# Kernel tuning notes

Hardware: AMD Instinct MI355X
Metric: run time of the kernel (lower is better)

## Reference

```python
import jax, jax.numpy as jnp
import numpy as np
from functools import partial

B, S, H, L, NH, V, A, NL = 64, 256, 768, 12, 12, 30522, 64, 2
HD = H // NH
EPS = 1e-12


def _ln(x, s, b):
    m = jnp.mean(x, axis=-1, keepdims=True)
    v = jnp.mean((x - m) ** 2, axis=-1, keepdims=True)
    return (x - m) * jax.lax.rsqrt(v + EPS) * s + b


def setup_inputs() -> dict:
    key = jax.random.key(0)
    ks = jax.random.split(key, 16)
    sc = 0.02
    inp = {
        'input_ids': jax.random.randint(ks[0], (B, S), 0, V, dtype=jnp.int32),
        'attention_mask': jnp.ones((B, S), dtype=jnp.int32),
        'token_type_ids': jnp.zeros((B, S), dtype=jnp.int32),
        'annotator_idx': jax.random.randint(ks[1], (B,), 0, A, dtype=jnp.int32),
        'word_emb': jax.random.normal(ks[2], (V, H), jnp.float32) * sc,
        'pos_emb': jax.random.normal(ks[3], (512, H), jnp.float32) * sc,
        'type_emb': jax.random.normal(ks[4], (2, H), jnp.float32) * sc,
        'emb_ln_s': jnp.ones((H,), jnp.float32),
        'emb_ln_b': jnp.zeros((H,), jnp.float32),
        'Wq': jax.random.normal(ks[5], (L, H, H), jnp.float32) * sc,
        'bq': jnp.zeros((L, H), jnp.float32),
        'Wk': jax.random.normal(ks[6], (L, H, H), jnp.float32) * sc,
        'bk': jnp.zeros((L, H), jnp.float32),
        'Wv': jax.random.normal(ks[7], (L, H, H), jnp.float32) * sc,
        'bv': jnp.zeros((L, H), jnp.float32),
        'Wo': jax.random.normal(ks[8], (L, H, H), jnp.float32) * sc,
        'bo': jnp.zeros((L, H), jnp.float32),
        'ln1_s': jnp.ones((L, H), jnp.float32),
        'ln1_b': jnp.zeros((L, H), jnp.float32),
        'W1': jax.random.normal(ks[9], (L, H, 4 * H), jnp.float32) * sc,
        'b1': jnp.zeros((L, 4 * H), jnp.float32),
        'W2': jax.random.normal(ks[10], (L, 4 * H, H), jnp.float32) * sc,
        'b2': jnp.zeros((L, H), jnp.float32),
        'ln2_s': jnp.ones((L, H), jnp.float32),
        'ln2_b': jnp.zeros((L, H), jnp.float32),
        'head_W': jax.random.normal(ks[11], (A, H, NL), jnp.float32) * sc,
        'head_b': jnp.zeros((A, NL), jnp.float32),
    }
    return inp


def _bert_forward(input_ids, attention_mask, token_type_ids, word_emb, pos_emb,
                  type_emb, emb_ln_s, emb_ln_b, layer_params):
    # embeddings
    h = word_emb[input_ids] + pos_emb[:S][None, :, :] + type_emb[token_type_ids]
    h = _ln(h, emb_ln_s, emb_ln_b)
    # additive attention bias from mask: [B,1,1,S]
    mask_bias = (1.0 - attention_mask.astype(h.dtype))[:, None, None, :] * -10000.0
    scale = 1.0 / np.sqrt(HD)

    def layer(h, p):
        Wq, bq, Wk, bk, Wv, bv, Wo, bo, l1s, l1b, W1, b1, W2, b2, l2s, l2b = p
        def heads(x, W, b):  # [B,S,H] -> [B,NH,S,HD]
            y = x @ W + b
            return y.reshape(B, S, NH, HD).transpose(0, 2, 1, 3)
        q = heads(h, Wq, bq)
        k = heads(h, Wk, bk)
        v = heads(h, Wv, bv)
        scores = jnp.einsum('bhqd,bhkd->bhqk', q, k) * scale + mask_bias
        attn = jax.nn.softmax(scores, axis=-1)
        ctx = jnp.einsum('bhqk,bhkd->bhqd', attn, v)
        ctx = ctx.transpose(0, 2, 1, 3).reshape(B, S, H)
        h = _ln(h + ctx @ Wo + bo, l1s, l1b)
        ffn = jax.nn.gelu(h @ W1 + b1, approximate=False) @ W2 + b2
        h = _ln(h + ffn, l2s, l2b)
        return h, None

    h, _ = jax.lax.scan(layer, h, layer_params)
    return h


def reference(input_ids, attention_mask, token_type_ids, annotator_idx,
              word_emb, pos_emb, type_emb, emb_ln_s, emb_ln_b,
              Wq, bq, Wk, bk, Wv, bv, Wo, bo, ln1_s, ln1_b,
              W1, b1, W2, b2, ln2_s, ln2_b, head_W, head_b):
    layer_params = (Wq, bq, Wk, bk, Wv, bv, Wo, bo, ln1_s, ln1_b,
                    W1, b1, W2, b2, ln2_s, ln2_b)
    h = _bert_forward(input_ids, attention_mask, token_type_ids, word_emb,
                      pos_emb, type_emb, emb_ln_s, emb_ln_b, layer_params)
    cls = h[:, 0, :]  # [B,H]
    # per-sample annotator-head routing: gather head weights, batched matvec
    logits = jnp.einsum('bh,bhl->bl', cls, head_W[annotator_idx]) + head_b[annotator_idx]
    return logits
```

## Files before the change

kernel.cpp:

```cpp
#include <hip/hip_runtime.h>

#define L_ 12
#define H_ 768
#define S_ 256
#define B_ 64
#define NH_ 12
#define HD_ 64
#define FF_ 3072
#define M_ (B_*S_)
#define QKVN (3*H_)

using bf16x8 = __attribute__((ext_vector_type(8))) __bf16;
using floatx4 = __attribute__((ext_vector_type(4))) float;

typedef const __attribute__((address_space(1))) void* gptr_t;
typedef __attribute__((address_space(3))) void* sptr_t;

__device__ __forceinline__ void async_copy16(const void* g, void* s) {
  __builtin_amdgcn_global_load_lds((gptr_t)g, (sptr_t)s, 16, 0, 0);
}

__device__ __forceinline__ unsigned short f2bf(float f) {
  unsigned int u = __float_as_uint(f);
  u += 0x7fffu + ((u >> 16) & 1u);
  return (unsigned short)(u >> 16);
}
__device__ __forceinline__ float bf2f(unsigned short s) {
  return __uint_as_float(((unsigned int)s) << 16);
}

__device__ __forceinline__ float gelu_f(float x) {
  float y = 0.7978845608f * (x + 0.044715f * x * x * x);
  float t = 1.0f - 2.0f / (1.0f + __expf(2.0f * y));
  return 0.5f * x * (1.0f + t);
}

__global__ __launch_bounds__(256) void transpose_bf16_kernel(
    const float* __restrict__ W, unsigned short* __restrict__ Wt, int K, int N) {
  __shared__ unsigned short t[64][65];
  const int n0 = blockIdx.x * 64, k0 = blockIdx.y * 64;
  const int tid = threadIdx.x;
#pragma unroll
  for (int p = 0; p < 16; ++p) {
    int idx = p * 256 + tid;
    int r = idx >> 6, c = idx & 63;
    t[r][c] = f2bf(W[(size_t)(k0 + r) * N + n0 + c]);
  }
  __syncthreads();
#pragma unroll
  for (int p = 0; p < 16; ++p) {
    int idx = p * 256 + tid;
    int r = idx >> 6, c = idx & 63;
    Wt[(size_t)(n0 + r) * K + k0 + c] = t[c][r];
  }
}

__global__ __launch_bounds__(256) void v_transpose_kernel(
    const unsigned short* __restrict__ qkv, unsigned short* __restrict__ vT) {
  const int st = blockIdx.x, bh = blockIdx.y;
  const int b = bh / NH_, nh = bh % NH_;
  __shared__ unsigned short t[64][65];
  const int tid = threadIdx.x;
  const int s0 = st * 64;
  const size_t rowbase = (size_t)b * S_ * QKVN + 2 * H_ + nh * 64;
#pragma unroll
  for (int p = 0; p < 16; ++p) {
    int idx = p * 256 + tid;
    int r = idx >> 6, c = idx & 63;
    t[r][c] = qkv[rowbase + (size_t)(s0 + r) * QKVN + c];
  }
  __syncthreads();
#pragma unroll
  for (int p = 0; p < 16; ++p) {
    int idx = p * 256 + tid;
    int r = idx >> 6, c = idx & 63;
    vT[((size_t)bh * 64 + r) * 256 + s0 + c] = t[c][r];
  }
}

__global__ __launch_bounds__(256) void qkv_bias_kernel(
    const float* __restrict__ bq, const float* __restrict__ bk,
    const float* __restrict__ bv, float* __restrict__ out) {
  int i = blockIdx.x * 256 + threadIdx.x;
  if (i >= L_ * QKVN) return;
  int l = i / QKVN, j = i % QKVN;
  float v;
  if (j < H_) v = bq[l * H_ + j];
  else if (j < 2 * H_) v = bk[l * H_ + j - H_];
  else v = bv[l * H_ + j - 2 * H_];
  out[i] = v;
}

__global__ __launch_bounds__(256) void embed_ln_kernel(
    const int* __restrict__ ids, const int* __restrict__ tts,
    const float* __restrict__ wemb, const float* __restrict__ pemb,
    const float* __restrict__ temb, const float* __restrict__ lns,
    const float* __restrict__ lnb, float* __restrict__ h,
    unsigned short* __restrict__ hbf) {
  const int tk = blockIdx.x;
  const int s = tk & (S_ - 1);
  const int tid = threadIdx.x;
  const int id = ids[tk];
  const int tt = tts[tk];
  float v[3];
#pragma unroll
  for (int i = 0; i < 3; ++i) {
    int j = tid + i * 256;
    v[i] = wemb[(size_t)id * H_ + j] + pemb[(size_t)s * H_ + j] + temb[(size_t)tt * H_ + j];
  }
  float sum = v[0] + v[1] + v[2];
  float ssq = v[0] * v[0] + v[1] * v[1] + v[2] * v[2];
#pragma unroll
  for (int off = 32; off; off >>= 1) {
    sum += __shfl_down(sum, off);
    ssq += __shfl_down(ssq, off);
  }
  __shared__ float rs[4], rq[4];
  const int lane = tid & 63, wid = tid >> 6;
  if (lane == 0) { rs[wid] = sum; rq[wid] = ssq; }
  __syncthreads();
  const float S = rs[0] + rs[1] + rs[2] + rs[3];
  const float Q = rq[0] + rq[1] + rq[2] + rq[3];
  const float mean = S * (1.0f / 768.0f);
  const float var = Q * (1.0f / 768.0f) - mean * mean;
  const float r = rsqrtf(var + 1e-12f);
#pragma unroll
  for (int i = 0; i < 3; ++i) {
    int j = tid + i * 256;
    float y = (v[i] - mean) * r * lns[j] + lnb[j];
    h[(size_t)tk * H_ + j] = y;
    hbf[(size_t)tk * H_ + j] = f2bf(y);
  }
}

__global__ __launch_bounds__(256) void residual_ln_kernel(
    const float* __restrict__ hin, const unsigned short* __restrict__ delta,
    const float* __restrict__ lns, const float* __restrict__ lnb,
    float* __restrict__ hout, unsigned short* __restrict__ hbf) {
  const int row = blockIdx.x;
  const int tid = threadIdx.x;
  float v[3];
#pragma unroll
  for (int i = 0; i < 3; ++i) {
    int j = tid + i * 256;
    v[i] = hin[(size_t)row * H_ + j] + bf2f(delta[(size_t)row * H_ + j]);
  }
  float sum = v[0] + v[1] + v[2];
  float ssq = v[0] * v[0] + v[1] * v[1] + v[2] * v[2];
#pragma unroll
  for (int off = 32; off; off >>= 1) {
    sum += __shfl_down(sum, off);
    ssq += __shfl_down(ssq, off);
  }
  __shared__ float rs[4], rq[4];
  const int lane = tid & 63, wid = tid >> 6;
  if (lane == 0) { rs[wid] = sum; rq[wid] = ssq; }
  __syncthreads();
  const float S = rs[0] + rs[1] + rs[2] + rs[3];
  const float Q = rq[0] + rq[1] + rq[2] + rq[3];
  const float mean = S * (1.0f / 768.0f);
  const float var = Q * (1.0f / 768.0f) - mean * mean;
  const float r = rsqrtf(var + 1e-12f);
#pragma unroll
  for (int i = 0; i < 3; ++i) {
    int j = tid + i * 256;
    float y = (v[i] - mean) * r * lns[j] + lnb[j];
    hout[(size_t)row * H_ + j] = y;
    hbf[(size_t)row * H_ + j] = f2bf(y);
  }
}

enum { EPI_BF16 = 0, EPI_GELU = 1, EPI_F32 = 2 };

#define BAR() asm volatile("s_barrier" ::: "memory")
#define WAIT_LGKM0() do { asm volatile("s_waitcnt lgkmcnt(0)" ::: "memory"); \
                          __builtin_amdgcn_sched_barrier(0); } while (0)
#define VM_WAIT(n) asm volatile("s_waitcnt vmcnt(" #n ")" ::: "memory")

#define GEMM_TILE(T_, DOSTAGE_, VMASM_)                                        \
  {                                                                            \
    const int slot_ = (T_) & 3;                                                \
    const unsigned short* Ab_ = &AS[slot_ * 8192] + aoff;                      \
    const unsigned short* Bb_ = &BS[slot_ * 8192] + boff;                      \
    bf16x8 af_[4], bf_[4];                                                     \
    _Pragma("unroll") for (int i_ = 0; i_ < 4; ++i_)                           \
        af_[i_] = *(const bf16x8*)(Ab_ + i_ * 512);                            \
    _Pragma("unroll") for (int j_ = 0; j_ < 4; ++j_)                           \
        bf_[j_] = *(const bf16x8*)(Bb_ + j_ * 512);                            \
    if (DOSTAGE_) {                                                            \
      const int ns_ = ((T_) + 3) & 3;                                          \
      const unsigned short* g_ = agp + (size_t)((T_) + 3) * 32;                \
      async_copy16(g_, asw + ns_ * 8192);                                      \
      async_copy16(g_ + (size_t)128 * K, asw + ns_ * 8192 + 4096);             \
    }                                                                          \
    BAR();                                                                     \
    WAIT_LGKM0();                                                              \
    __builtin_amdgcn_s_setprio(1);                                             \
    _Pragma("unroll") for (int i_ = 0; i_ < 4; ++i_)                           \
      _Pragma("unroll") for (int j_ = 0; j_ < 4; ++j_)                         \
        acc[i_][j_] = __builtin_amdgcn_mfma_f32_16x16x32_bf16(                 \
            bf_[j_], af_[i_], acc[i_][j_], 0, 0, 0);                           \
    __builtin_amdgcn_s_setprio(0);                                             \
    BAR();                                                                     \
    _Pragma("unroll") for (int i_ = 0; i_ < 4; ++i_)                           \
        af_[i_] = *(const bf16x8*)(Ab_ + 2048 + i_ * 512);                     \
    if (DOSTAGE_) {                                                            \
      const int ns_ = ((T_) + 3) & 3;                                          \
      const unsigned short* g_ = bgp + (size_t)((T_) + 3) * 32;                \
      async_copy16(g_, bsw + ns_ * 8192);                                      \
      async_copy16(g_ + (size_t)128 * K, bsw + ns_ * 8192 + 4096);             \
    }                                                                          \
    VMASM_;                                                                    \
    BAR();                                                                     \
    WAIT_LGKM0();                                                              \
    __builtin_amdgcn_s_setprio(1);                                             \
    _Pragma("unroll") for (int i_ = 0; i_ < 4; ++i_)                           \
      _Pragma("unroll") for (int j_ = 0; j_ < 4; ++j_)                         \
        acc[4 + i_][j_] = __builtin_amdgcn_mfma_f32_16x16x32_bf16(             \
            bf_[j_], af_[i_], acc[4 + i_][j_], 0, 0, 0);                       \
    __builtin_amdgcn_s_setprio(0);                                             \
    BAR();                                                                     \
  }

template <int EPI>
__global__ __launch_bounds__(512, 2) void gemm256_kernel(
    const unsigned short* __restrict__ A, const unsigned short* __restrict__ Bt,
    const float* __restrict__ bias, void* __restrict__ Cv,
    int M, int N, int K) {
  __shared__ __align__(128) unsigned short AS[4 * 8192];
  __shared__ __align__(128) unsigned short BS[4 * 8192];
  (void)M;
  const int NT = K >> 5;

  const int nwg = (int)gridDim.x;
  const int nbx = N >> 8;
  const int cpx = nwg >> 3;
  const int bid = (int)blockIdx.x;
  const int swz = (bid & 7) * cpx + (bid >> 3);
  const int n0 = (swz % nbx) << 8;
  const int m0 = (swz / nbx) << 8;

  const int tid = threadIdx.x;
  const int wave = tid >> 6;
  const int lane = tid & 63;
  const int lr = lane & 15;
  const int quad = lane >> 4;
  const int wgm = wave & 1;
  const int wgn = wave >> 1;

  const int aoff = (wgm * 128 + lr) * 32 + quad * 8;
  const int boff = (wgn * 64 + lr) * 32 + quad * 8;

  const unsigned short* __restrict__ agp =
      A + (size_t)(m0 + wave * 16 + (lane >> 2)) * K + (lane & 3) * 8;
  const unsigned short* __restrict__ bgp =
      Bt + (size_t)(n0 + wave * 16 + (lane >> 2)) * K + (lane & 3) * 8;
  unsigned short* asw = &AS[wave * 512];
  unsigned short* bsw = &BS[wave * 512];

  floatx4 acc[8][4] = {};

#pragma unroll
  for (int u = 0; u < 3; ++u) {
    const unsigned short* ga = agp + (size_t)u * 32;
    const unsigned short* gb = bgp + (size_t)u * 32;
    async_copy16(ga, asw + u * 8192);
    async_copy16(ga + (size_t)128 * K, asw + u * 8192 + 4096);
    async_copy16(gb, bsw + u * 8192);
    async_copy16(gb + (size_t)128 * K, bsw + u * 8192 + 4096);
  }
  VM_WAIT(8);
  BAR();

  for (int t = 0; t < NT - 3; ++t) GEMM_TILE(t, true, VM_WAIT(8));
  GEMM_TILE(NT - 3, false, VM_WAIT(4));
  GEMM_TILE(NT - 2, false, VM_WAIT(0));
  GEMM_TILE(NT - 1, false, (void)0);

#pragma unroll
  for (int j = 0; j < 4; ++j) {
    const int nb = n0 + wgn * 64 + j * 16 + quad * 4;
    const float4 bv = *(const float4*)&bias[nb];
#pragma unroll
    for (int i = 0; i < 8; ++i) {
      const int m = m0 + wgm * 128 + i * 16 + lr;
      float v0 = acc[i][j][0] + bv.x;
      float v1 = acc[i][j][1] + bv.y;
      float v2 = acc[i][j][2] + bv.z;
      float v3 = acc[i][j][3] + bv.w;
      if (EPI == EPI_GELU) {
        v0 = gelu_f(v0); v1 = gelu_f(v1); v2 = gelu_f(v2); v3 = gelu_f(v3);
      }
      if (EPI == EPI_F32) {
        float4 o = make_float4(v0, v1, v2, v3);
        *(float4*)&((float*)Cv)[(size_t)m * N + nb] = o;
      } else {
        uint2 o;
        o.x = (unsigned)f2bf(v0) | ((unsigned)f2bf(v1) << 16);
        o.y = (unsigned)f2bf(v2) | ((unsigned)f2bf(v3) << 16);
        *(uint2*)&((unsigned short*)Cv)[(size_t)m * N + nb] = o;
      }
    }
  }
}

__global__ __launch_bounds__(256, 2) void flash_attn_kernel(
    const unsigned short* __restrict__ qkv, const unsigned short* __restrict__ vT,
    const int* __restrict__ mask, unsigned short* __restrict__ ctx) {
  const int bh = blockIdx.x;
  const int b = bh / NH_, nh = bh % NH_;
  __shared__ __align__(16) unsigned short Ks[64 * 64];
  __shared__ __align__(16) unsigned short Vs[64 * 64];
  __shared__ __align__(16) unsigned short Ps[4][64 * 66];
  __shared__ float bias_s[256];
  const int tid = threadIdx.x;
  const int wave = tid >> 6, lane = tid & 63;
  const int lr = lane & 15, quad = lane >> 4;
  bias_s[tid] = (1.0f - (float)mask[b * S_ + tid]) * -10000.0f;

  const size_t rowbase = (size_t)b * S_ * QKVN;
  const int q0 = wave * 64;

  bf16x8 qf[4][2];
#pragma unroll
  for (int i = 0; i < 4; ++i)
#pragma unroll
    for (int kc = 0; kc < 2; ++kc)
      qf[i][kc] = *(const bf16x8*)&qkv[rowbase + (size_t)(q0 + i * 16 + lr) * QKVN +
                                       nh * 64 + kc * 32 + quad * 8];

  floatx4 o[4][4] = {};
  float mrow[4][4], lrow[4][4];
#pragma unroll
  for (int i = 0; i < 4; ++i)
#pragma unroll
    for (int r = 0; r < 4; ++r) { mrow[i][r] = -1e30f; lrow[i][r] = 0.f; }

  const size_t vbase = (size_t)bh * 64 * 256;

  for (int jt = 0; jt < S_; jt += 64) {
    __syncthreads();
#pragma unroll
    for (int p = 0; p < 2; ++p) {
      int cid = p * 256 + wave * 64 + lane;
      int row = cid >> 3, c = cid & 7;
      async_copy16(&qkv[rowbase + (size_t)(jt + row) * QKVN + H_ + nh * 64 + c * 8],
                   &Ks[(p * 256 + wave * 64) * 8]);
      async_copy16(&vT[vbase + (size_t)row * 256 + jt + c * 8],
                   &Vs[(p * 256 + wave * 64) * 8]);
    }
    __syncthreads();

    floatx4 s[4][4];
#pragma unroll
    for (int jn = 0; jn < 4; ++jn) {
      bf16x8 kf0 = *(const bf16x8*)&Ks[(jn * 16 + lr) * 64 + quad * 8];
      bf16x8 kf1 = *(const bf16x8*)&Ks[(jn * 16 + lr) * 64 + 32 + quad * 8];
#pragma unroll
      for (int i = 0; i < 4; ++i) {
        floatx4 a = {};
        a = __builtin_amdgcn_mfma_f32_16x16x32_bf16(qf[i][0], kf0, a, 0, 0, 0);
        a = __builtin_amdgcn_mfma_f32_16x16x32_bf16(qf[i][1], kf1, a, 0, 0, 0);
        s[i][jn] = a;
      }
    }
    float bj[4];
#pragma unroll
    for (int jn = 0; jn < 4; ++jn) bj[jn] = bias_s[jt + jn * 16 + lr];
#pragma unroll
    for (int i = 0; i < 4; ++i)
#pragma unroll
      for (int jn = 0; jn < 4; ++jn)
#pragma unroll
        for (int r = 0; r < 4; ++r)
          s[i][jn][r] = s[i][jn][r] * 0.125f + bj[jn];

#pragma unroll
    for (int i = 0; i < 4; ++i) {
#pragma unroll
      for (int r = 0; r < 4; ++r) {
        float mx = fmaxf(fmaxf(s[i][0][r], s[i][1][r]), fmaxf(s[i][2][r], s[i][3][r]));
        mx = fmaxf(mx, __shfl_xor(mx, 1));
        mx = fmaxf(mx, __shfl_xor(mx, 2));
        mx = fmaxf(mx, __shfl_xor(mx, 4));
        mx = fmaxf(mx, __shfl_xor(mx, 8));
        float mn = fmaxf(mrow[i][r], mx);
        float alpha = __expf(mrow[i][r] - mn);
        mrow[i][r] = mn;
        float ps = 0.f;
#pragma unroll
        for (int jn = 0; jn < 4; ++jn) {
          float pv = __expf(s[i][jn][r] - mn);
          s[i][jn][r] = pv;
          ps += pv;
        }
        ps += __shfl_xor(ps, 1);
        ps += __shfl_xor(ps, 2);
        ps += __shfl_xor(ps, 4);
        ps += __shfl_xor(ps, 8);
        lrow[i][r] = lrow[i][r] * alpha + ps;
#pragma unroll
        for (int n = 0; n < 4; ++n) o[i][n][r] *= alpha;
      }
    }

#pragma unroll
    for (int i = 0; i < 4; ++i)
#pragma unroll
      for (int jn = 0; jn < 4; ++jn)
#pragma unroll
        for (int r = 0; r < 4; ++r)
          Ps[wave][(i * 16 + quad * 4 + r) * 66 + jn * 16 + lr] = f2bf(s[i][jn][r]);
    __syncthreads();

#pragma unroll
    for (int kc = 0; kc < 2; ++kc) {
      bf16x8 pf[4], vf[4];
#pragma unroll
      for (int i = 0; i < 4; ++i)
        pf[i] = *(const bf16x8*)&Ps[wave][(i * 16 + lr) * 66 + kc * 32 + quad * 8];
#pragma unroll
      for (int n = 0; n < 4; ++n)
        vf[n] = *(const bf16x8*)&Vs[(n * 16 + lr) * 64 + kc * 32 + quad * 8];
#pragma unroll
      for (int i = 0; i < 4; ++i)
#pragma unroll
        for (int n = 0; n < 4; ++n)
          o[i][n] = __builtin_amdgcn_mfma_f32_16x16x32_bf16(pf[i], vf[n], o[i][n], 0, 0, 0);
    }
  }

#pragma unroll
  for (int i = 0; i < 4; ++i) {
#pragma unroll
    for (int r = 0; r < 4; ++r) {
      float inv = 1.0f / lrow[i][r];
      int row = b * S_ + q0 + i * 16 + quad * 4 + r;
#pragma unroll
      for (int n = 0; n < 4; ++n)
        ctx[(size_t)row * H_ + nh * 64 + n * 16 + lr] = f2bf(o[i][n][r] * inv);
    }
  }
}

__global__ __launch_bounds__(256) void head_kernel(
    const float* __restrict__ h, const int* __restrict__ aidx,
    const float* __restrict__ hW, const float* __restrict__ hb,
    float* __restrict__ out) {
  const int b = blockIdx.x;
  const int a = aidx[b];
  const float* cls = h + (size_t)b * S_ * H_;
  const float* w = hW + (size_t)a * H_ * 2;
  float a0 = 0.f, a1 = 0.f;
  for (int j = threadIdx.x; j < H_; j += 256) {
    float c = cls[j];
    a0 += c * w[j * 2];
    a1 += c * w[j * 2 + 1];
  }
#pragma unroll
  for (int off = 32; off; off >>= 1) {
    a0 += __shfl_down(a0, off);
    a1 += __shfl_down(a1, off);
  }
  __shared__ float r0[4], r1[4];
  const int lane = threadIdx.x & 63, wid = threadIdx.x >> 6;
  if (lane == 0) { r0[wid] = a0; r1[wid] = a1; }
  __syncthreads();
  if (threadIdx.x == 0) {
    out[b * 2 + 0] = r0[0] + r0[1] + r0[2] + r0[3] + hb[a * 2 + 0];
    out[b * 2 + 1] = r1[0] + r1[1] + r1[2] + r1[3] + hb[a * 2 + 1];
  }
}

extern "C" void kernel_launch(void* const* d_in, const int* in_sizes, int n_in,
                              void* d_out, int out_size, void* d_ws, size_t ws_size,
                              hipStream_t stream) {
  const int* input_ids = (const int*)d_in[0];
  const int* attn_mask = (const int*)d_in[1];
  const int* type_ids = (const int*)d_in[2];
  const int* aidx = (const int*)d_in[3];
  const float* wemb = (const float*)d_in[4];
  const float* pemb = (const float*)d_in[5];
  const float* temb = (const float*)d_in[6];
  const float* elns = (const float*)d_in[7];
  const float* elnb = (const float*)d_in[8];
  const float* Wq = (const float*)d_in[9];
  const float* bq = (const float*)d_in[10];
  const float* Wk = (const float*)d_in[11];
  const float* bk = (const float*)d_in[12];
  const float* Wv = (const float*)d_in[13];
  const float* bv = (const float*)d_in[14];
  const float* Wo = (const float*)d_in[15];
  const float* bo = (const float*)d_in[16];
  const float* ln1s = (const float*)d_in[17];
  const float* ln1b = (const float*)d_in[18];
  const float* W1 = (const float*)d_in[19];
  const float* b1 = (const float*)d_in[20];
  const float* W2 = (const float*)d_in[21];
  const float* b2 = (const float*)d_in[22];
  const float* ln2s = (const float*)d_in[23];
  const float* ln2b = (const float*)d_in[24];
  const float* hW = (const float*)d_in[25];
  const float* hb = (const float*)d_in[26];
  float* out = (float*)d_out;
  (void)in_sizes; (void)n_in; (void)out_size; (void)ws_size;

  char* p = (char*)d_ws;
  float* h = (float*)p;              p += (size_t)M_ * H_ * 4;
  unsigned short* delta = (unsigned short*)p;  p += (size_t)M_ * H_ * 4;
  unsigned short* hbf = (unsigned short*)p;   p += (size_t)M_ * H_ * 2;
  unsigned short* qkv = (unsigned short*)p;   p += (size_t)M_ * QKVN * 2;
  unsigned short* ctx = (unsigned short*)p;   p += (size_t)M_ * H_ * 2;
  unsigned short* ffn1 = qkv;
  unsigned short* wbuf = (unsigned short*)p;  p += (size_t)7077888 * 2;
  float* qkvbias = (float*)p;        p += (size_t)L_ * QKVN * 4;
  unsigned short* vT = delta;

  unsigned short* Wqkv_t = wbuf;
  unsigned short* Wo_t = wbuf + (size_t)QKVN * H_;
  unsigned short* W1_t = Wo_t + (size_t)H_ * H_;
  unsigned short* W2_t = W1_t + (size_t)H_ * FF_;

  qkv_bias_kernel<<<(L_ * QKVN + 255) / 256, 256, 0, stream>>>(bq, bk, bv, qkvbias);
  embed_ln_kernel<<<M_, 256, 0, stream>>>(input_ids, type_ids, wemb, pemb, temb,
                                          elns, elnb, h, hbf);

  for (int l = 0; l < L_; ++l) {
    const size_t HH = (size_t)H_ * H_;
    const size_t HF = (size_t)H_ * FF_;
    transpose_bf16_kernel<<<dim3(12, 12), 256, 0, stream>>>(Wq + l * HH, Wqkv_t, H_, H_);
    transpose_bf16_kernel<<<dim3(12, 12), 256, 0, stream>>>(Wk + l * HH, Wqkv_t + HH, H_, H_);
    transpose_bf16_kernel<<<dim3(12, 12), 256, 0, stream>>>(Wv + l * HH, Wqkv_t + 2 * HH, H_, H_);
    transpose_bf16_kernel<<<dim3(12, 12), 256, 0, stream>>>(Wo + l * HH, Wo_t, H_, H_);
    transpose_bf16_kernel<<<dim3(48, 12), 256, 0, stream>>>(W1 + l * HF, W1_t, H_, FF_);
    transpose_bf16_kernel<<<dim3(12, 48), 256, 0, stream>>>(W2 + l * HF, W2_t, FF_, H_);

    gemm256_kernel<EPI_BF16><<<dim3((QKVN / 256) * (M_ / 256)), 512, 0, stream>>>(
        hbf, Wqkv_t, qkvbias + (size_t)l * QKVN, qkv, M_, QKVN, H_);
    v_transpose_kernel<<<dim3(4, B_ * NH_), 256, 0, stream>>>(qkv, vT);
    flash_attn_kernel<<<B_ * NH_, 256, 0, stream>>>(qkv, vT, attn_mask, ctx);
    gemm256_kernel<EPI_BF16><<<dim3((H_ / 256) * (M_ / 256)), 512, 0, stream>>>(
        ctx, Wo_t, bo + (size_t)l * H_, delta, M_, H_, H_);
    residual_ln_kernel<<<M_, 256, 0, stream>>>(h, delta, ln1s + (size_t)l * H_,
                                               ln1b + (size_t)l * H_, h, hbf);
    gemm256_kernel<EPI_GELU><<<dim3((FF_ / 256) * (M_ / 256)), 512, 0, stream>>>(
        hbf, W1_t, b1 + (size_t)l * FF_, ffn1, M_, FF_, H_);
    gemm256_kernel<EPI_BF16><<<dim3((H_ / 256) * (M_ / 256)), 512, 0, stream>>>(
        ffn1, W2_t, b2 + (size_t)l * H_, delta, M_, H_, FF_);
    residual_ln_kernel<<<M_, 256, 0, stream>>>(h, delta, ln2s + (size_t)l * H_,
                                               ln2b + (size_t)l * H_, h, hbf);
  }

  head_kernel<<<B_, 256, 0, stream>>>(h, aidx, hW, hb, out);
}
```

Measured before the change: 6.697 ms.

## Replace 256x256 GEMM with 128x128 tile, 3-stage pipeline, and XOR-swizzled LDS

The 512-thread GEMM with a 256x256 output tile and four-stage async LDS pipeline is replaced by a 256-thread kernel with a 128x128 tile, three pipeline stages and three blocks per CU. LDS rows are XOR-swizzled on both the async-copy write side and the fragment read side to avoid bank conflicts. The aim is more workgroups, better wave coverage on small-N GEMMs (768 columns), and less LDS per block. The cost is lower arithmetic intensity per tile and more global traffic for A and B.

Result: faster. 5.830 ms (-12.9%).

```diff
diff --git a/kernel.cpp b/kernel.cpp
--- a/kernel.cpp
+++ b/kernel.cpp
@@ -177,22 +177,24 @@
                           __builtin_amdgcn_sched_barrier(0); } while (0)
 #define VM_WAIT(n) asm volatile("s_waitcnt vmcnt(" #n ")" ::: "memory")
 
-#define GEMM_TILE(T_, DOSTAGE_, VMASM_)                                        \
+#define GEMM128_TILE(T_, SLOT_, NSLOT_, DOSTAGE_, VMASM_)                      \
   {                                                                            \
-    const int slot_ = (T_) & 3;                                                \
-    const unsigned short* Ab_ = &AS[slot_ * 8192] + aoff;                      \
-    const unsigned short* Bb_ = &BS[slot_ * 8192] + boff;                      \
+    const unsigned short* Ab_ = &AS[(SLOT_) * 4096];                           \
+    const unsigned short* Bb_ = &BS[(SLOT_) * 4096];                           \
     bf16x8 af_[4], bf_[4];                                                     \
     _Pragma("unroll") for (int i_ = 0; i_ < 4; ++i_)                           \
-        af_[i_] = *(const bf16x8*)(Ab_ + i_ * 512);                            \
+        af_[i_] = *(const bf16x8*)(Ab_ + aoff + i_ * 512);                     \
     _Pragma("unroll") for (int j_ = 0; j_ < 4; ++j_)                           \
-        bf_[j_] = *(const bf16x8*)(Bb_ + j_ * 512);                            \
+        bf_[j_] = *(const bf16x8*)(Bb_ + boff + j_ * 512);                     \
     if (DOSTAGE_) {                                                            \
-      const int ns_ = ((T_) + 3) & 3;                                          \
-      const unsigned short* g_ = agp + (size_t)((T_) + 3) * 32;                \
-      async_copy16(g_, asw + ns_ * 8192);                                      \
-      async_copy16(g_ + (size_t)128 * K, asw + ns_ * 8192 + 4096);             \
+      const unsigned short* ga_ = agp + (size_t)((T_) + 2) * 32;               \
+      const unsigned short* gb_ = bgp + (size_t)((T_) + 2) * 32;               \
+      _Pragma("unroll") for (int u_ = 0; u_ < 2; ++u_) {                       \
+        async_copy16(ga_ + (size_t)u_ * 64 * K, asw + (NSLOT_) * 4096 + u_ * 2048); \
+        async_copy16(gb_ + (size_t)u_ * 64 * K, bsw + (NSLOT_) * 4096 + u_ * 2048); \
+      }                                                                        \
     }                                                                          \
+    VMASM_;                                                                    \
     BAR();                                                                     \
     WAIT_LGKM0();                                                              \
     __builtin_amdgcn_s_setprio(1);                                             \
@@ -202,43 +204,25 @@
             bf_[j_], af_[i_], acc[i_][j_], 0, 0, 0);                           \
     __builtin_amdgcn_s_setprio(0);                                             \
     BAR();                                                                     \
-    _Pragma("unroll") for (int i_ = 0; i_ < 4; ++i_)                           \
-        af_[i_] = *(const bf16x8*)(Ab_ + 2048 + i_ * 512);                     \
-    if (DOSTAGE_) {                                                            \
-      const int ns_ = ((T_) + 3) & 3;                                          \
-      const unsigned short* g_ = bgp + (size_t)((T_) + 3) * 32;                \
-      async_copy16(g_, bsw + ns_ * 8192);                                      \
-      async_copy16(g_ + (size_t)128 * K, bsw + ns_ * 8192 + 4096);             \
-    }                                                                          \
-    VMASM_;                                                                    \
-    BAR();                                                                     \
-    WAIT_LGKM0();                                                              \
-    __builtin_amdgcn_s_setprio(1);                                             \
-    _Pragma("unroll") for (int i_ = 0; i_ < 4; ++i_)                           \
-      _Pragma("unroll") for (int j_ = 0; j_ < 4; ++j_)                         \
-        acc[4 + i_][j_] = __builtin_amdgcn_mfma_f32_16x16x32_bf16(             \
-            bf_[j_], af_[i_], acc[4 + i_][j_], 0, 0, 0);                       \
-    __builtin_amdgcn_s_setprio(0);                                             \
-    BAR();                                                                     \
   }
 
 template <int EPI>
-__global__ __launch_bounds__(512, 2) void gemm256_kernel(
+__global__ __launch_bounds__(256, 3) void gemm128p_kernel(
     const unsigned short* __restrict__ A, const unsigned short* __restrict__ Bt,
     const float* __restrict__ bias, void* __restrict__ Cv,
     int M, int N, int K) {
-  __shared__ __align__(128) unsigned short AS[4 * 8192];
-  __shared__ __align__(128) unsigned short BS[4 * 8192];
+  __shared__ __align__(128) unsigned short AS[3 * 4096];
+  __shared__ __align__(128) unsigned short BS[3 * 4096];
   (void)M;
   const int NT = K >> 5;
 
   const int nwg = (int)gridDim.x;
-  const int nbx = N >> 8;
+  const int nbx = N >> 7;
   const int cpx = nwg >> 3;
   const int bid = (int)blockIdx.x;
   const int swz = (bid & 7) * cpx + (bid >> 3);
-  const int n0 = (swz % nbx) << 8;
-  const int m0 = (swz / nbx) << 8;
+  const int n0 = (swz % nbx) << 7;
+  const int m0 = (swz / nbx) << 7;
 
   const int tid = threadIdx.x;
   const int wave = tid >> 6;
@@ -248,42 +232,51 @@
   const int wgm = wave & 1;
   const int wgn = wave >> 1;
 
-  const int aoff = (wgm * 128 + lr) * 32 + quad * 8;
-  const int boff = (wgn * 64 + lr) * 32 + quad * 8;
-
-  const unsigned short* __restrict__ agp =
-      A + (size_t)(m0 + wave * 16 + (lane >> 2)) * K + (lane & 3) * 8;
-  const unsigned short* __restrict__ bgp =
-      Bt + (size_t)(n0 + wave * 16 + (lane >> 2)) * K + (lane & 3) * 8;
+  const int colx = (quad ^ ((lr >> 1) & 3)) * 8;
+  const int aoff = (wgm * 64 + lr) * 32 + colx;
+  const int boff = (wgn * 64 + lr) * 32 + colx;
+
+  const int srow = wave * 16 + (lane >> 2);
+  const int scol = ((lane & 3) ^ ((lane >> 3) & 3)) * 8;
+  const unsigned short* __restrict__ agp = A + (size_t)(m0 + srow) * K + scol;
+  const unsigned short* __restrict__ bgp = Bt + (size_t)(n0 + srow) * K + scol;
   unsigned short* asw = &AS[wave * 512];
   unsigned short* bsw = &BS[wave * 512];
 
-  floatx4 acc[8][4] = {};
-
-#pragma unroll
-  for (int u = 0; u < 3; ++u) {
-    const unsigned short* ga = agp + (size_t)u * 32;
-    const unsigned short* gb = bgp + (size_t)u * 32;
-    async_copy16(ga, asw + u * 8192);
-    async_copy16(ga + (size_t)128 * K, asw + u * 8192 + 4096);
-    async_copy16(gb, bsw + u * 8192);
-    async_copy16(gb + (size_t)128 * K, bsw + u * 8192 + 4096);
-  }
-  VM_WAIT(8);
+  floatx4 acc[4][4] = {};
+
+#pragma unroll
+  for (int t0 = 0; t0 < 2; ++t0) {
+    const unsigned short* ga = agp + (size_t)t0 * 32;
+    const unsigned short* gb = bgp + (size_t)t0 * 32;
+#pragma unroll
+    for (int u = 0; u < 2; ++u) {
+      async_copy16(ga + (size_t)u * 64 * K, asw + t0 * 4096 + u * 2048);
+      async_copy16(gb + (size_t)u * 64 * K, bsw + t0 * 4096 + u * 2048);
+    }
+  }
+  VM_WAIT(4);
   BAR();
 
-  for (int t = 0; t < NT - 3; ++t) GEMM_TILE(t, true, VM_WAIT(8));
-  GEMM_TILE(NT - 3, false, VM_WAIT(4));
-  GEMM_TILE(NT - 2, false, VM_WAIT(0));
-  GEMM_TILE(NT - 1, false, (void)0);
+  int sl = 0;
+  int t = 0;
+  for (; t < NT - 2; ++t) {
+    const int ns = (sl >= 1) ? sl - 1 : 2;
+    GEMM128_TILE(t, sl, ns, true, VM_WAIT(4));
+    sl = (sl == 2) ? 0 : sl + 1;
+  }
+  GEMM128_TILE(t, sl, 0, false, VM_WAIT(0));
+  sl = (sl == 2) ? 0 : sl + 1;
+  ++t;
+  GEMM128_TILE(t, sl, 0, false, (void)0);
 
 #pragma unroll
   for (int j = 0; j < 4; ++j) {
     const int nb = n0 + wgn * 64 + j * 16 + quad * 4;
     const float4 bv = *(const float4*)&bias[nb];
 #pragma unroll
-    for (int i = 0; i < 8; ++i) {
-      const int m = m0 + wgm * 128 + i * 16 + lr;
+    for (int i = 0; i < 4; ++i) {
+      const int m = m0 + wgm * 64 + i * 16 + lr;
       float v0 = acc[i][j][0] + bv.x;
       float v1 = acc[i][j][1] + bv.y;
       float v2 = acc[i][j][2] + bv.z;
@@ -535,17 +528,17 @@
     transpose_bf16_kernel<<<dim3(48, 12), 256, 0, stream>>>(W1 + l * HF, W1_t, H_, FF_);
     transpose_bf16_kernel<<<dim3(12, 48), 256, 0, stream>>>(W2 + l * HF, W2_t, FF_, H_);
 
-    gemm256_kernel<EPI_BF16><<<dim3((QKVN / 256) * (M_ / 256)), 512, 0, stream>>>(
+    gemm128p_kernel<EPI_BF16><<<dim3((QKVN / 128) * (M_ / 128)), 256, 0, stream>>>(
         hbf, Wqkv_t, qkvbias + (size_t)l * QKVN, qkv, M_, QKVN, H_);
     v_transpose_kernel<<<dim3(4, B_ * NH_), 256, 0, stream>>>(qkv, vT);
     flash_attn_kernel<<<B_ * NH_, 256, 0, stream>>>(qkv, vT, attn_mask, ctx);
-    gemm256_kernel<EPI_BF16><<<dim3((H_ / 256) * (M_ / 256)), 512, 0, stream>>>(
+    gemm128p_kernel<EPI_BF16><<<dim3((H_ / 128) * (M_ / 128)), 256, 0, stream>>>(
         ctx, Wo_t, bo + (size_t)l * H_, delta, M_, H_, H_);
     residual_ln_kernel<<<M_, 256, 0, stream>>>(h, delta, ln1s + (size_t)l * H_,
                                                ln1b + (size_t)l * H_, h, hbf);
-    gemm256_kernel<EPI_GELU><<<dim3((FF_ / 256) * (M_ / 256)), 512, 0, stream>>>(
+    gemm128p_kernel<EPI_GELU><<<dim3((FF_ / 128) * (M_ / 128)), 256, 0, stream>>>(
         hbf, W1_t, b1 + (size_t)l * FF_, ffn1, M_, FF_, H_);
-    gemm256_kernel<EPI_BF16><<<dim3((H_ / 256) * (M_ / 256)), 512, 0, stream>>>(
+    gemm128p_kernel<EPI_BF16><<<dim3((H_ / 128) * (M_ / 128)), 256, 0, stream>>>(
         ffn1, W2_t, b2 + (size_t)l * H_, delta, M_, H_, FF_);
     residual_ln_kernel<<<M_, 256, 0, stream>>>(h, delta, ln2s + (size_t)l * H_,
                                                ln2b + (size_t)l * H_, h, hbf);
```
